# Kernel optimization log

Measured on AMD Instinct MI355X. Metric: run time of the kernel, lower is better.

Reference implementation:

```python
import jax, jax.numpy as jnp
import numpy as np

EPS = 1e-5  # BatchNorm2d default eps


def conv1x1_bn(x, W, gamma, beta, mean, var):
    # 1x1 conv (no bias) + BatchNorm2d in inference form.
    # x: (n, Cin, h, w), W: (Cout, Cin)
    y = jnp.einsum('oc,nchw->nohw', W, x)
    inv = gamma / jnp.sqrt(var + EPS)          # (C,)
    return y * inv[None, :, None, None] + (beta - mean * inv)[None, :, None, None]


def setup_inputs() -> dict:
    key = jax.random.key(0)
    ks = jax.random.split(key, 16)
    B, C, H, W = 8, 256, 128, 128
    sd = 1.0 / np.sqrt(C)
    inp = {
        'x':  jax.random.normal(ks[0], (B, C, H, W), jnp.float32),
        'Wk': jax.random.normal(ks[1], (C, C), jnp.float32) * sd,
        'k_gamma': jax.random.uniform(ks[2], (C,), jnp.float32, 0.5, 1.5),
        'k_beta':  jax.random.normal(ks[3], (C,), jnp.float32) * 0.1,
        'k_mean':  jax.random.normal(ks[4], (C,), jnp.float32) * 0.1,
        'k_var':   jax.random.uniform(ks[5], (C,), jnp.float32, 0.5, 1.5),
        'Wq': jax.random.normal(ks[6], (C, C), jnp.float32) * sd,
        'q_gamma': jax.random.uniform(ks[7], (C,), jnp.float32, 0.5, 1.5),
        'q_beta':  jax.random.normal(ks[8], (C,), jnp.float32) * 0.1,
        'q_mean':  jax.random.normal(ks[9], (C,), jnp.float32) * 0.1,
        'q_var':   jax.random.uniform(ks[10], (C,), jnp.float32, 0.5, 1.5),
        'Wv': jax.random.normal(ks[11], (C, C), jnp.float32) * sd,
        'v_gamma': jax.random.uniform(ks[12], (C,), jnp.float32, 0.5, 1.5),
        'v_beta':  jax.random.normal(ks[13], (C,), jnp.float32) * 0.1,
        'v_mean':  jax.random.normal(ks[14], (C,), jnp.float32) * 0.1,
        'v_var':   jax.random.uniform(ks[15], (C,), jnp.float32, 0.5, 1.5),
    }
    return inp


def reference(x, Wk, k_gamma, k_beta, k_mean, k_var,
              Wq, q_gamma, q_beta, q_mean, q_var,
              Wv, v_gamma, v_beta, v_mean, v_var):
    n, c, h, w = x.shape
    k = conv1x1_bn(x, Wk, k_gamma, k_beta, k_mean, k_var).reshape(n, c, h * w)  # (n,C,S)
    q = conv1x1_bn(x, Wq, q_gamma, q_beta, q_mean, q_var).reshape(n, c, h * w)
    v = conv1x1_bn(x, Wv, v_gamma, v_beta, v_mean, v_var).reshape(n, c, h * w)
    # torch: attention = softmax(q @ k^T, dim=2) -> (n, C, C) channel attention
    attn = jax.nn.softmax(jnp.einsum('ncs,nds->ncd', q, k), axis=-1)
    out = jnp.einsum('ncd,nds->ncs', attn, v).reshape(n, c, h, w)
    return out + x  # res = Identity (in_channels == out_channels)
```

## Files before the change

### kernel.cpp

```cpp
#include <hip/hip_runtime.h>


typedef __bf16 bf16x8 __attribute__((ext_vector_type(8)));
typedef float f32x4 __attribute__((ext_vector_type(4)));
typedef unsigned short us8 __attribute__((ext_vector_type(8)));

#define EPS 1e-5f

__device__ __forceinline__ unsigned short f2bf(float f) {
  unsigned int u = __float_as_uint(f);
  u += 0x7fffu + ((u >> 16) & 1u);
  return (unsigned short)(u >> 16);
}
__device__ __forceinline__ float bf2f(unsigned short h) {
  return __uint_as_float(((unsigned int)h) << 16);
}
__device__ __forceinline__ bf16x8 ld_frag(const unsigned short* p) {
  union { us8 u; bf16x8 b; } x;
  x.u = *(const us8*)p;
  return x.b;
}

#define LDBS 40

#define CONV_WRITE                                                          \
  _Pragma("unroll")                                                         \
  for (int u = 0; u < 4; ++u) {                                             \
    float fv[8] = {pa[u].x, pa[u].y, pa[u].z, pa[u].w,                      \
                   pb[u].x, pb[u].y, pb[u].z, pb[u].w};                     \
    union { unsigned short s[8]; uint4 v; } H, L;                           \
    _Pragma("unroll")                                                       \
    for (int e = 0; e < 8; ++e) {                                           \
      const unsigned short hh = f2bf(fv[e]);                                \
      H.s[e] = hh;                                                          \
      L.s[e] = f2bf(2.0f * (fv[e] - bf2f(hh)));                             \
      rs[u] += fv[e];                                                       \
    }                                                                       \
    *(uint4*)&sh[(srow + u * 64) * LDBS + sg * 8] = H.v;                    \
    *(uint4*)&sl[(srow + u * 64) * LDBS + sg * 8] = L.v;                    \
  }

__global__ __launch_bounds__(256, 2) void kGram(const float* __restrict__ x,
                                                float* __restrict__ Gp,
                                                float* __restrict__ rp,
                                                int chunk) {
  __shared__ __align__(16) unsigned short sh[256 * LDBS];
  __shared__ __align__(16) unsigned short sl[256 * LDBS];
  const int n = blockIdx.z, h = blockIdx.y;
  const int k0 = blockIdx.x * chunk;
  const int nkt = chunk >> 5;
  const int tid = threadIdx.x;
  const float* xn = x + (size_t)n * 4194304;

  f32x4 acc[4][8];
  const f32x4 z4 = {0.f, 0.f, 0.f, 0.f};
#pragma unroll
  for (int i = 0; i < 4; ++i)
#pragma unroll
    for (int j = 0; j < 8; ++j) acc[i][j] = z4;
  float rs[4] = {0.f, 0.f, 0.f, 0.f};

  const int lane = tid & 63, w = tid >> 6;
  const int m = lane & 15, q = lane >> 4;
  const int wr = w >> 1, wc = w & 1;
  const int srow = tid >> 2, sg = tid & 3;

  float4 pa[4], pb[4];

#pragma unroll
  for (int u = 0; u < 4; ++u) {
    const float* p = xn + (size_t)(srow + u * 64) * 16384 + k0 + sg * 8;
    pa[u] = *(const float4*)p;
    pb[u] = *(const float4*)(p + 4);
  }

  for (int kt = 0; kt < nkt; ++kt) {
    if (kt) __syncthreads();
    CONV_WRITE
    __syncthreads();
    if (kt + 1 < nkt) {
      const int kb = k0 + (kt + 1) * 32;
#pragma unroll
      for (int u = 0; u < 4; ++u) {
        const float* p = xn + (size_t)(srow + u * 64) * 16384 + kb + sg * 8;
        pa[u] = *(const float4*)p;
        pb[u] = *(const float4*)(p + 4);
      }
    }
    bf16x8 Ah[4];
#pragma unroll
    for (int i = 0; i < 4; ++i)
      Ah[i] = ld_frag(&sh[(h * 128 + wr * 64 + i * 16 + m) * LDBS + q * 8]);
#pragma unroll
    for (int j = 0; j < 8; ++j) {
      const int off = (wc * 128 + j * 16 + m) * LDBS + q * 8;
      const bf16x8 Bh = ld_frag(&sh[off]);
      const bf16x8 Bl = ld_frag(&sl[off]);
#pragma unroll
      for (int i = 0; i < 4; ++i) {
        acc[i][j] = __builtin_amdgcn_mfma_f32_16x16x32_bf16(Ah[i], Bh, acc[i][j], 0, 0, 0);
        acc[i][j] = __builtin_amdgcn_mfma_f32_16x16x32_bf16(Ah[i], Bl, acc[i][j], 0, 0, 0);
      }
    }
  }

  const size_t slot = (size_t)n * gridDim.x + blockIdx.x;
  if (h == 0) {
#pragma unroll
    for (int u = 0; u < 4; ++u) {
      float v = rs[u];
      v += __shfl_xor(v, 1);
      v += __shfl_xor(v, 2);
      if ((lane & 3) == 0) rp[slot * 256 + (srow + u * 64)] = v;
    }
  }
  float* Gpn = Gp + slot * 65536;
#pragma unroll
  for (int i = 0; i < 4; ++i)
#pragma unroll
    for (int j = 0; j < 8; ++j)
#pragma unroll
      for (int e = 0; e < 4; ++e) {
        const int grow = h * 128 + wr * 64 + i * 16 + q * 4 + e;
        const int gcol = wc * 128 + j * 16 + m;
        Gpn[grow * 256 + gcol] = 0.5f * acc[i][j][e];
      }
}

__global__ void kReduce(float* __restrict__ Gp, int splits) {
  const int e4 = (blockIdx.x * 256 + threadIdx.x) * 4;
  const int n = e4 >> 16, el = e4 & 65535;
  float* p = Gp + (size_t)n * splits * 65536 + el;
  float4 s = {0.f, 0.f, 0.f, 0.f};
  for (int i = 0; i < splits; ++i) {
    const float4 v = *(const float4*)(p + (size_t)i * 65536);
    s.x += v.x; s.y += v.y; s.z += v.z; s.w += v.w;
  }
  *(float4*)p = s;
}

__global__ void kSym(const float* __restrict__ Gs, float* __restrict__ G,
                     int sstride) {
  __shared__ __align__(16) float pt[64][68];
  const int n = blockIdx.y;
  const int bi = blockIdx.x >> 2, bj = blockIdx.x & 3;
  const float* gsn = Gs + (size_t)n * sstride;
  float* gn = G + (size_t)n * 65536;
  const int t = threadIdx.x, r = t >> 2, cg = (t & 3) * 16;
#pragma unroll
  for (int e = 0; e < 16; e += 4)
    *(float4*)&pt[r][cg + e] =
        *(const float4*)(gsn + (size_t)(bj * 64 + r) * 256 + bi * 64 + cg + e);
  __syncthreads();
#pragma unroll
  for (int e = 0; e < 16; e += 4) {
    const float4 a =
        *(const float4*)(gsn + (size_t)(bi * 64 + r) * 256 + bj * 64 + cg + e);
    float4 o;
    o.x = a.x + pt[cg + e + 0][r];
    o.y = a.y + pt[cg + e + 1][r];
    o.z = a.z + pt[cg + e + 2][r];
    o.w = a.w + pt[cg + e + 3][r];
    *(float4*)(gn + (size_t)(bi * 64 + r) * 256 + bj * 64 + cg + e) = o;
  }
}

#define TLD 260
__global__ __launch_bounds__(256) void kAttn(
    const float* __restrict__ G, const float* __restrict__ rp, int splits,
    const float* __restrict__ Wq, const float* __restrict__ qga, const float* __restrict__ qbe,
    const float* __restrict__ qme, const float* __restrict__ qva,
    const float* __restrict__ Wk, const float* __restrict__ kga, const float* __restrict__ kbe,
    const float* __restrict__ kme, const float* __restrict__ kva,
    const float* __restrict__ Wv, const float* __restrict__ vga, const float* __restrict__ vbe,
    const float* __restrict__ vme, const float* __restrict__ vva,
    unsigned short* __restrict__ M, float* __restrict__ cvec) {
  __shared__ __align__(16) float t_lds[8 * TLD];
  __shared__ __align__(16) float p_lds[8 * TLD];
  __shared__ __align__(16) float r_lds[256];
  __shared__ float ivv_lds[256], bv_lds[256];
  __shared__ float rq_lds[8], bq_lds[8], rsum_lds[8];

  const int n = blockIdx.y, r0 = blockIdx.x * 8;
  const int t = threadIdx.x;
  const int lane = t & 63;
  const int w = __builtin_amdgcn_readfirstlane(t >> 6);
  const float* Gn = G + (size_t)n * 65536;

  {
    float s = 0.f;
    const float* p = rp + (size_t)n * splits * 256 + t;
    for (int ss = 0; ss < splits; ++ss) s += p[ss * 256];
    r_lds[t] = s;
    const float iv = vga[t] * rsqrtf(vva[t] + EPS);
    ivv_lds[t] = iv;
    bv_lds[t] = vbe[t] - vme[t] * iv;
  }
  __syncthreads();

  const int c0 = r0 + 2 * w, c1 = c0 + 1;
  const float ivq0 = qga[c0] * rsqrtf(qva[c0] + EPS);
  const float ivq1 = qga[c1] * rsqrtf(qva[c1] + EPS);

  {
    const float4 r4 = *(const float4*)(r_lds + lane * 4);
#pragma unroll
    for (int rr = 0; rr < 2; ++rr) {
      const float4 w4 = *(const float4*)(Wq + (size_t)(c0 + rr) * 256 + lane * 4);
      float s = w4.x * r4.x + w4.y * r4.y + w4.z * r4.z + w4.w * r4.w;
      s += __shfl_xor(s, 1);  s += __shfl_xor(s, 2);  s += __shfl_xor(s, 4);
      s += __shfl_xor(s, 8);  s += __shfl_xor(s, 16); s += __shfl_xor(s, 32);
      if (lane == 0) rq_lds[2 * w + rr] = s * (rr ? ivq1 : ivq0);
    }
    if (lane == 0) {
      bq_lds[2 * w + 0] = qbe[c0] - qme[c0] * ivq0;
      bq_lds[2 * w + 1] = qbe[c1] - qme[c1] * ivq1;
    }
  }

  {
    float4 tr0 = {0.f, 0.f, 0.f, 0.f}, tr1 = {0.f, 0.f, 0.f, 0.f};
    const float* wq0 = Wq + (size_t)c0 * 256;
    const float* wq1 = Wq + (size_t)c1 * 256;
    for (int kb = 0; kb < 256; kb += 4) {
      union { float4 v; float f[4]; } A0, A1;
      A0.v = *(const float4*)(wq0 + kb);
      A1.v = *(const float4*)(wq1 + kb);
#pragma unroll
      for (int e = 0; e < 4; ++e) {
        const float4 g4 = *(const float4*)(Gn + (size_t)(kb + e) * 256 + lane * 4);
        const float a0 = A0.f[e], a1 = A1.f[e];
        tr0.x += a0 * g4.x; tr0.y += a0 * g4.y; tr0.z += a0 * g4.z; tr0.w += a0 * g4.w;
        tr1.x += a1 * g4.x; tr1.y += a1 * g4.y; tr1.z += a1 * g4.z; tr1.w += a1 * g4.w;
      }
    }
    tr0.x *= ivq0; tr0.y *= ivq0; tr0.z *= ivq0; tr0.w *= ivq0;
    tr1.x *= ivq1; tr1.y *= ivq1; tr1.z *= ivq1; tr1.w *= ivq1;
    *(float4*)(t_lds + (2 * w + 0) * TLD + lane * 4) = tr0;
    *(float4*)(t_lds + (2 * w + 1) * TLD + lane * 4) = tr1;
  }
  __syncthreads();

  {
    float lreg[8];
#pragma unroll
    for (int i = 0; i < 8; ++i) lreg[i] = 0.f;
    const float ivk = kga[t] * rsqrtf(kva[t] + EPS);
    const float bkd = kbe[t] - kme[t] * ivk;
    float rkd = 0.f;
    const float* wkrow = Wk + (size_t)t * 256;
    for (int jb = 0; jb < 256; jb += 4) {
      const float4 w4 = *(const float4*)(wkrow + jb);
      const float4 r4 = *(const float4*)(r_lds + jb);
      rkd += w4.x * r4.x + w4.y * r4.y + w4.z * r4.z + w4.w * r4.w;
#pragma unroll
      for (int i = 0; i < 8; ++i) {
        const float4 t4 = *(const float4*)(t_lds + i * TLD + jb);
        lreg[i] += t4.x * w4.x + t4.y * w4.y + t4.z * w4.z + t4.w * w4.w;
      }
    }
#pragma unroll
    for (int i = 0; i < 8; ++i)
      p_lds[i * TLD + t] = ivk * lreg[i] + rq_lds[i] * bkd +
                           bq_lds[i] * (ivk * rkd) + 16384.0f * bq_lds[i] * bkd;
  }
  __syncthreads();

  {
    const int i = t >> 5, s = t & 31;
    float* row = p_lds + i * TLD;
    float mx = -1e30f;
#pragma unroll
    for (int u = 0; u < 8; ++u) mx = fmaxf(mx, row[s + u * 32]);
    mx = fmaxf(mx, __shfl_xor(mx, 1));
    mx = fmaxf(mx, __shfl_xor(mx, 2));
    mx = fmaxf(mx, __shfl_xor(mx, 4));
    mx = fmaxf(mx, __shfl_xor(mx, 8));
    mx = fmaxf(mx, __shfl_xor(mx, 16));
    float sraw = 0.f, sbv = 0.f;
#pragma unroll
    for (int u = 0; u < 8; ++u) {
      const int d = s + u * 32;
      const float e = __expf(row[d] - mx);
      sraw += e;
      sbv += e * bv_lds[d];
      row[d] = e * ivv_lds[d];
    }
    sraw += __shfl_xor(sraw, 1);  sbv += __shfl_xor(sbv, 1);
    sraw += __shfl_xor(sraw, 2);  sbv += __shfl_xor(sbv, 2);
    sraw += __shfl_xor(sraw, 4);  sbv += __shfl_xor(sbv, 4);
    sraw += __shfl_xor(sraw, 8);  sbv += __shfl_xor(sbv, 8);
    sraw += __shfl_xor(sraw, 16); sbv += __shfl_xor(sbv, 16);
    if (s == 0) {
      rsum_lds[i] = sraw;
      cvec[n * 256 + r0 + i] = sbv / sraw;
    }
  }
  __syncthreads();

  {
    float mreg[8];
#pragma unroll
    for (int i = 0; i < 8; ++i) mreg[i] = 0.f;
    for (int db = 0; db < 256; db += 4) {
      float wv[4];
#pragma unroll
      for (int e = 0; e < 4; ++e) wv[e] = Wv[(size_t)(db + e) * 256 + t];
#pragma unroll
      for (int i = 0; i < 8; ++i) {
        const float4 p4 = *(const float4*)(p_lds + i * TLD + db);
        mreg[i] += p4.x * wv[0] + p4.y * wv[1] + p4.z * wv[2] + p4.w * wv[3];
      }
    }
#pragma unroll
    for (int i = 0; i < 8; ++i)
      M[((size_t)n * 256 + r0 + i) * 256 + t] = f2bf(mreg[i] / rsum_lds[i]);
  }
}

#define LDT 40
__global__ __launch_bounds__(256, 2) void kOut(const float* __restrict__ x,
                                               const unsigned short* __restrict__ M,
                                               const float* __restrict__ cvec,
                                               float* __restrict__ out) {
  __shared__ __align__(16) unsigned short xt[64 * LDT];
  __shared__ __align__(16) float xf[256 * 64];
  const int n = blockIdx.y, s0 = blockIdx.x * 64;
  const int tid = threadIdx.x;
  const float* xn = x + (size_t)n * 4194304;
  const unsigned short* Mn = M + (size_t)n * 65536;
  const int lane = tid & 63, w = tid >> 6;
  const int m = lane & 15, q = lane >> 4;
  const int ch0 = tid >> 4, f0 = tid & 15;

  f32x4 acc[4][4];
  const f32x4 z4 = {0.f, 0.f, 0.f, 0.f};
#pragma unroll
  for (int i = 0; i < 4; ++i)
#pragma unroll
    for (int ct = 0; ct < 4; ++ct) acc[i][ct] = z4;

  float4 pv[2];
#pragma unroll
  for (int u = 0; u < 2; ++u)
    pv[u] = *(const float4*)(xn + (size_t)(ch0 + u * 16) * 16384 + s0 + f0 * 4);

  for (int kt = 0; kt < 8; ++kt) {
    if (kt) __syncthreads();
#pragma unroll
    for (int u = 0; u < 2; ++u) {
      const int ch = kt * 32 + ch0 + u * 16;
      const float4 v = pv[u];
      *(float4*)&xf[ch * 64 + f0 * 4] = v;
      xt[(f0 * 4 + 0) * LDT + ch - kt * 32] = f2bf(v.x);
      xt[(f0 * 4 + 1) * LDT + ch - kt * 32] = f2bf(v.y);
      xt[(f0 * 4 + 2) * LDT + ch - kt * 32] = f2bf(v.z);
      xt[(f0 * 4 + 3) * LDT + ch - kt * 32] = f2bf(v.w);
    }
    bf16x8 A[4];
#pragma unroll
    for (int i = 0; i < 4; ++i)
      A[i] = ld_frag(&Mn[((w * 4 + i) * 16 + m) * 256 + kt * 32 + q * 8]);
    __syncthreads();
    if (kt < 7) {
#pragma unroll
      for (int u = 0; u < 2; ++u)
        pv[u] = *(const float4*)(xn + (size_t)((kt + 1) * 32 + ch0 + u * 16) * 16384 + s0 + f0 * 4);
    }
    bf16x8 B[4];
#pragma unroll
    for (int ct = 0; ct < 4; ++ct)
      B[ct] = ld_frag(&xt[(ct * 16 + m) * LDT + q * 8]);
#pragma unroll
    for (int i = 0; i < 4; ++i)
#pragma unroll
      for (int ct = 0; ct < 4; ++ct)
        acc[i][ct] = __builtin_amdgcn_mfma_f32_16x16x32_bf16(A[i], B[ct], acc[i][ct], 0, 0, 0);
  }
#pragma unroll
  for (int i = 0; i < 4; ++i) {
    const int cb = w * 64 + i * 16 + q * 4;
#pragma unroll
    for (int e = 0; e < 4; ++e) {
      const int c = cb + e;
      const float cv = cvec[n * 256 + c];
      float* orow = out + ((size_t)n * 256 + c) * 16384 + s0;
#pragma unroll
      for (int ct = 0; ct < 4; ++ct) {
        const int s = ct * 16 + m;
        orow[s] = acc[i][ct][e] + cv + xf[c * 64 + s];
      }
    }
  }
}

extern "C" void kernel_launch(void* const* d_in, const int* in_sizes, int n_in,
                              void* d_out, int out_size, void* d_ws, size_t ws_size,
                              hipStream_t stream) {
  const float* x   = (const float*)d_in[0];
  const float* Wk  = (const float*)d_in[1];
  const float* kga = (const float*)d_in[2];
  const float* kbe = (const float*)d_in[3];
  const float* kme = (const float*)d_in[4];
  const float* kva = (const float*)d_in[5];
  const float* Wq  = (const float*)d_in[6];
  const float* qga = (const float*)d_in[7];
  const float* qbe = (const float*)d_in[8];
  const float* qme = (const float*)d_in[9];
  const float* qva = (const float*)d_in[10];
  const float* Wv  = (const float*)d_in[11];
  const float* vga = (const float*)d_in[12];
  const float* vbe = (const float*)d_in[13];
  const float* vme = (const float*)d_in[14];
  const float* vva = (const float*)d_in[15];

  char* ws = (char*)d_ws;
  float* G           = (float*)(ws);
  unsigned short* Mm = (unsigned short*)(ws + 2097152);
  float* cv          = (float*)(ws + 3145728);
  float* rp          = (float*)(ws + 3153920);
  float* Gp          = (float*)(ws + 3416064);
  float* out         = (float*)d_out;

  int splits = 32;
  while (splits > 1 &&
         (size_t)3416064 + (size_t)splits * 8 * 65536 * 4 > ws_size)
    splits >>= 1;
  const int chunk = 16384 / splits;

  kGram<<<dim3(splits, 2, 8), 256, 0, stream>>>(x, Gp, rp, chunk);
  kReduce<<<512, 256, 0, stream>>>(Gp, splits);
  kSym<<<dim3(16, 8), 256, 0, stream>>>(Gp, G, splits * 65536);
  kAttn<<<dim3(32, 8), 256, 0, stream>>>(G, rp, splits,
                                         Wq, qga, qbe, qme, qva,
                                         Wk, kga, kbe, kme, kva,
                                         Wv, vga, vbe, vme, vva,
                                         Mm, cv);
  kOut<<<dim3(256, 8), 256, 0, stream>>>(x, Mm, cv, out);
}
```

Measured before the change: 388.1 us.

## Fuse split reduction with symmetrization, halve attention rows per block, vectorize output stores

Merges the split-sum reduction and the transpose-add symmetrization into a single kernel that walks only upper-triangular 64x64 tile pairs, removing one launch and one full pass over the partial Gram buffer. The attention kernel now handles 4 rows per block instead of 8, doubling the grid to improve occupancy, at the cost of more redundant loads of G, Wk and Wv. The output kernel swaps the MFMA operand order so each lane holds 4 consecutive spatial positions, allowing float4 stores and float4 residual reads. The fused reduce uses only 80 blocks, each serially summing all splits, so it has less parallelism than the old 512-block reduction.

```diff
diff --git a/kernel.cpp b/kernel.cpp
--- a/kernel.cpp
+++ b/kernel.cpp
@@ -127,41 +127,60 @@
       }
 }
 
-__global__ void kReduce(float* __restrict__ Gp, int splits) {
-  const int e4 = (blockIdx.x * 256 + threadIdx.x) * 4;
-  const int n = e4 >> 16, el = e4 & 65535;
-  float* p = Gp + (size_t)n * splits * 65536 + el;
-  float4 s = {0.f, 0.f, 0.f, 0.f};
-  for (int i = 0; i < splits; ++i) {
-    const float4 v = *(const float4*)(p + (size_t)i * 65536);
-    s.x += v.x; s.y += v.y; s.z += v.z; s.w += v.w;
-  }
-  *(float4*)p = s;
-}
-
-__global__ void kSym(const float* __restrict__ Gs, float* __restrict__ G,
-                     int sstride) {
-  __shared__ __align__(16) float pt[64][68];
-  const int n = blockIdx.y;
-  const int bi = blockIdx.x >> 2, bj = blockIdx.x & 3;
-  const float* gsn = Gs + (size_t)n * sstride;
+__global__ void kRedSym(const float* __restrict__ Gp, float* __restrict__ G,
+                        int splits) {
+  __shared__ __align__(16) float tl[64][68];
+  const int n = blockIdx.y, p = blockIdx.x;
+  const int bi = p < 4 ? 0 : p < 7 ? 1 : p < 9 ? 2 : 3;
+  const int bj = p < 4 ? p : p < 7 ? p - 3 : p < 9 ? p - 5 : 3;
+  const int t = threadIdx.x, r = t >> 2, cg = (t & 3) * 16;
+  float a[16], b[16];
+#pragma unroll
+  for (int e = 0; e < 16; ++e) { a[e] = 0.f; b[e] = 0.f; }
+  const float* base = Gp + (size_t)n * splits * 65536;
+  for (int s = 0; s < splits; ++s) {
+    const float* ps = base + (size_t)s * 65536;
+#pragma unroll
+    for (int e = 0; e < 16; e += 4) {
+      const float4 va = *(const float4*)(ps + (size_t)(bi * 64 + r) * 256 + bj * 64 + cg + e);
+      a[e] += va.x; a[e + 1] += va.y; a[e + 2] += va.z; a[e + 3] += va.w;
+      if (bi != bj) {
+        const float4 vb = *(const float4*)(ps + (size_t)(bj * 64 + r) * 256 + bi * 64 + cg + e);
+        b[e] += vb.x; b[e + 1] += vb.y; b[e + 2] += vb.z; b[e + 3] += vb.w;
+      }
+    }
+  }
+  if (bi == bj) {
+#pragma unroll
+    for (int e = 0; e < 16; ++e) b[e] = a[e];
+  }
   float* gn = G + (size_t)n * 65536;
-  const int t = threadIdx.x, r = t >> 2, cg = (t & 3) * 16;
-#pragma unroll
-  for (int e = 0; e < 16; e += 4)
-    *(float4*)&pt[r][cg + e] =
-        *(const float4*)(gsn + (size_t)(bj * 64 + r) * 256 + bi * 64 + cg + e);
+#pragma unroll
+  for (int e = 0; e < 16; ++e) tl[r][cg + e] = b[e];
   __syncthreads();
 #pragma unroll
   for (int e = 0; e < 16; e += 4) {
-    const float4 a =
-        *(const float4*)(gsn + (size_t)(bi * 64 + r) * 256 + bj * 64 + cg + e);
     float4 o;
-    o.x = a.x + pt[cg + e + 0][r];
-    o.y = a.y + pt[cg + e + 1][r];
-    o.z = a.z + pt[cg + e + 2][r];
-    o.w = a.w + pt[cg + e + 3][r];
+    o.x = a[e + 0] + tl[cg + e + 0][r];
+    o.y = a[e + 1] + tl[cg + e + 1][r];
+    o.z = a[e + 2] + tl[cg + e + 2][r];
+    o.w = a[e + 3] + tl[cg + e + 3][r];
     *(float4*)(gn + (size_t)(bi * 64 + r) * 256 + bj * 64 + cg + e) = o;
+  }
+  if (bi != bj) {
+    __syncthreads();
+#pragma unroll
+    for (int e = 0; e < 16; ++e) tl[r][cg + e] = a[e];
+    __syncthreads();
+#pragma unroll
+    for (int e = 0; e < 16; e += 4) {
+      float4 o;
+      o.x = b[e + 0] + tl[cg + e + 0][r];
+      o.y = b[e + 1] + tl[cg + e + 1][r];
+      o.z = b[e + 2] + tl[cg + e + 2][r];
+      o.w = b[e + 3] + tl[cg + e + 3][r];
+      *(float4*)(gn + (size_t)(bj * 64 + r) * 256 + bi * 64 + cg + e) = o;
+    }
   }
 }
 
@@ -175,13 +194,13 @@
     const float* __restrict__ Wv, const float* __restrict__ vga, const float* __restrict__ vbe,
     const float* __restrict__ vme, const float* __restrict__ vva,
     unsigned short* __restrict__ M, float* __restrict__ cvec) {
-  __shared__ __align__(16) float t_lds[8 * TLD];
-  __shared__ __align__(16) float p_lds[8 * TLD];
+  __shared__ __align__(16) float t_lds[4 * TLD];
+  __shared__ __align__(16) float p_lds[4 * TLD];
   __shared__ __align__(16) float r_lds[256];
   __shared__ float ivv_lds[256], bv_lds[256];
-  __shared__ float rq_lds[8], bq_lds[8], rsum_lds[8];
-
-  const int n = blockIdx.y, r0 = blockIdx.x * 8;
+  __shared__ float rq_lds[4], bq_lds[4], rsum_lds[4];
+
+  const int n = blockIdx.y, r0 = blockIdx.x * 4;
   const int t = threadIdx.x;
   const int lane = t & 63;
   const int w = __builtin_amdgcn_readfirstlane(t >> 6);
@@ -198,53 +217,43 @@
   }
   __syncthreads();
 
-  const int c0 = r0 + 2 * w, c1 = c0 + 1;
+  const int c0 = r0 + w;
   const float ivq0 = qga[c0] * rsqrtf(qva[c0] + EPS);
-  const float ivq1 = qga[c1] * rsqrtf(qva[c1] + EPS);
 
   {
     const float4 r4 = *(const float4*)(r_lds + lane * 4);
-#pragma unroll
-    for (int rr = 0; rr < 2; ++rr) {
-      const float4 w4 = *(const float4*)(Wq + (size_t)(c0 + rr) * 256 + lane * 4);
-      float s = w4.x * r4.x + w4.y * r4.y + w4.z * r4.z + w4.w * r4.w;
-      s += __shfl_xor(s, 1);  s += __shfl_xor(s, 2);  s += __shfl_xor(s, 4);
-      s += __shfl_xor(s, 8);  s += __shfl_xor(s, 16); s += __shfl_xor(s, 32);
-      if (lane == 0) rq_lds[2 * w + rr] = s * (rr ? ivq1 : ivq0);
-    }
+    const float4 w4 = *(const float4*)(Wq + (size_t)c0 * 256 + lane * 4);
+    float s = w4.x * r4.x + w4.y * r4.y + w4.z * r4.z + w4.w * r4.w;
+    s += __shfl_xor(s, 1);  s += __shfl_xor(s, 2);  s += __shfl_xor(s, 4);
+    s += __shfl_xor(s, 8);  s += __shfl_xor(s, 16); s += __shfl_xor(s, 32);
     if (lane == 0) {
-      bq_lds[2 * w + 0] = qbe[c0] - qme[c0] * ivq0;
-      bq_lds[2 * w + 1] = qbe[c1] - qme[c1] * ivq1;
-    }
-  }
-
-  {
-    float4 tr0 = {0.f, 0.f, 0.f, 0.f}, tr1 = {0.f, 0.f, 0.f, 0.f};
+      rq_lds[w] = s * ivq0;
+      bq_lds[w] = qbe[c0] - qme[c0] * ivq0;
+    }
+  }
+
+  {
+    float4 tr0 = {0.f, 0.f, 0.f, 0.f};
     const float* wq0 = Wq + (size_t)c0 * 256;
-    const float* wq1 = Wq + (size_t)c1 * 256;
     for (int kb = 0; kb < 256; kb += 4) {
-      union { float4 v; float f[4]; } A0, A1;
+      union { float4 v; float f[4]; } A0;
       A0.v = *(const float4*)(wq0 + kb);
-      A1.v = *(const float4*)(wq1 + kb);
 #pragma unroll
       for (int e = 0; e < 4; ++e) {
         const float4 g4 = *(const float4*)(Gn + (size_t)(kb + e) * 256 + lane * 4);
-        const float a0 = A0.f[e], a1 = A1.f[e];
+        const float a0 = A0.f[e];
         tr0.x += a0 * g4.x; tr0.y += a0 * g4.y; tr0.z += a0 * g4.z; tr0.w += a0 * g4.w;
-        tr1.x += a1 * g4.x; tr1.y += a1 * g4.y; tr1.z += a1 * g4.z; tr1.w += a1 * g4.w;
       }
     }
     tr0.x *= ivq0; tr0.y *= ivq0; tr0.z *= ivq0; tr0.w *= ivq0;
-    tr1.x *= ivq1; tr1.y *= ivq1; tr1.z *= ivq1; tr1.w *= ivq1;
-    *(float4*)(t_lds + (2 * w + 0) * TLD + lane * 4) = tr0;
-    *(float4*)(t_lds + (2 * w + 1) * TLD + lane * 4) = tr1;
+    *(float4*)(t_lds + w * TLD + lane * 4) = tr0;
   }
   __syncthreads();
 
   {
-    float lreg[8];
-#pragma unroll
-    for (int i = 0; i < 8; ++i) lreg[i] = 0.f;
+    float lreg[4];
+#pragma unroll
+    for (int i = 0; i < 4; ++i) lreg[i] = 0.f;
     const float ivk = kga[t] * rsqrtf(kva[t] + EPS);
     const float bkd = kbe[t] - kme[t] * ivk;
     float rkd = 0.f;
@@ -254,33 +263,34 @@
       const float4 r4 = *(const float4*)(r_lds + jb);
       rkd += w4.x * r4.x + w4.y * r4.y + w4.z * r4.z + w4.w * r4.w;
 #pragma unroll
-      for (int i = 0; i < 8; ++i) {
+      for (int i = 0; i < 4; ++i) {
         const float4 t4 = *(const float4*)(t_lds + i * TLD + jb);
         lreg[i] += t4.x * w4.x + t4.y * w4.y + t4.z * w4.z + t4.w * w4.w;
       }
     }
 #pragma unroll
-    for (int i = 0; i < 8; ++i)
+    for (int i = 0; i < 4; ++i)
       p_lds[i * TLD + t] = ivk * lreg[i] + rq_lds[i] * bkd +
                            bq_lds[i] * (ivk * rkd) + 16384.0f * bq_lds[i] * bkd;
   }
   __syncthreads();
 
   {
-    const int i = t >> 5, s = t & 31;
+    const int i = t >> 6, s = t & 63;
     float* row = p_lds + i * TLD;
     float mx = -1e30f;
 #pragma unroll
-    for (int u = 0; u < 8; ++u) mx = fmaxf(mx, row[s + u * 32]);
+    for (int u = 0; u < 4; ++u) mx = fmaxf(mx, row[s + u * 64]);
     mx = fmaxf(mx, __shfl_xor(mx, 1));
     mx = fmaxf(mx, __shfl_xor(mx, 2));
     mx = fmaxf(mx, __shfl_xor(mx, 4));
     mx = fmaxf(mx, __shfl_xor(mx, 8));
     mx = fmaxf(mx, __shfl_xor(mx, 16));
+    mx = fmaxf(mx, __shfl_xor(mx, 32));
     float sraw = 0.f, sbv = 0.f;
 #pragma unroll
-    for (int u = 0; u < 8; ++u) {
-      const int d = s + u * 32;
+    for (int u = 0; u < 4; ++u) {
+      const int d = s + u * 64;
       const float e = __expf(row[d] - mx);
       sraw += e;
       sbv += e * bv_lds[d];
@@ -291,6 +301,7 @@
     sraw += __shfl_xor(sraw, 4);  sbv += __shfl_xor(sbv, 4);
     sraw += __shfl_xor(sraw, 8);  sbv += __shfl_xor(sbv, 8);
     sraw += __shfl_xor(sraw, 16); sbv += __shfl_xor(sbv, 16);
+    sraw += __shfl_xor(sraw, 32); sbv += __shfl_xor(sbv, 32);
     if (s == 0) {
       rsum_lds[i] = sraw;
       cvec[n * 256 + r0 + i] = sbv / sraw;
@@ -299,21 +310,21 @@
   __syncthreads();
 
   {
-    float mreg[8];
-#pragma unroll
-    for (int i = 0; i < 8; ++i) mreg[i] = 0.f;
+    float mreg[4];
+#pragma unroll
+    for (int i = 0; i < 4; ++i) mreg[i] = 0.f;
     for (int db = 0; db < 256; db += 4) {
       float wv[4];
 #pragma unroll
       for (int e = 0; e < 4; ++e) wv[e] = Wv[(size_t)(db + e) * 256 + t];
 #pragma unroll
-      for (int i = 0; i < 8; ++i) {
+      for (int i = 0; i < 4; ++i) {
         const float4 p4 = *(const float4*)(p_lds + i * TLD + db);
         mreg[i] += p4.x * wv[0] + p4.y * wv[1] + p4.z * wv[2] + p4.w * wv[3];
       }
     }
 #pragma unroll
-    for (int i = 0; i < 8; ++i)
+    for (int i = 0; i < 4; ++i)
       M[((size_t)n * 256 + r0 + i) * 256 + t] = f2bf(mreg[i] / rsum_lds[i]);
   }
 }
@@ -375,21 +386,23 @@
     for (int i = 0; i < 4; ++i)
 #pragma unroll
       for (int ct = 0; ct < 4; ++ct)
-        acc[i][ct] = __builtin_amdgcn_mfma_f32_16x16x32_bf16(A[i], B[ct], acc[i][ct], 0, 0, 0);
+        acc[i][ct] = __builtin_amdgcn_mfma_f32_16x16x32_bf16(B[ct], A[i], acc[i][ct], 0, 0, 0);
   }
 #pragma unroll
   for (int i = 0; i < 4; ++i) {
-    const int cb = w * 64 + i * 16 + q * 4;
-#pragma unroll
-    for (int e = 0; e < 4; ++e) {
-      const int c = cb + e;
-      const float cv = cvec[n * 256 + c];
-      float* orow = out + ((size_t)n * 256 + c) * 16384 + s0;
-#pragma unroll
-      for (int ct = 0; ct < 4; ++ct) {
-        const int s = ct * 16 + m;
-        orow[s] = acc[i][ct][e] + cv + xf[c * 64 + s];
-      }
+    const int c = (w * 4 + i) * 16 + m;
+    const float cv = cvec[n * 256 + c];
+    float* orow = out + ((size_t)n * 256 + c) * 16384 + s0;
+#pragma unroll
+    for (int ct = 0; ct < 4; ++ct) {
+      const int sl = ct * 16 + q * 4;
+      const float4 xr = *(const float4*)&xf[c * 64 + sl];
+      float4 o;
+      o.x = acc[i][ct][0] + cv + xr.x;
+      o.y = acc[i][ct][1] + cv + xr.y;
+      o.z = acc[i][ct][2] + cv + xr.z;
+      o.w = acc[i][ct][3] + cv + xr.w;
+      *(float4*)(orow + sl) = o;
     }
   }
 }
@@ -429,9 +442,8 @@
   const int chunk = 16384 / splits;
 
   kGram<<<dim3(splits, 2, 8), 256, 0, stream>>>(x, Gp, rp, chunk);
-  kReduce<<<512, 256, 0, stream>>>(Gp, splits);
-  kSym<<<dim3(16, 8), 256, 0, stream>>>(Gp, G, splits * 65536);
-  kAttn<<<dim3(32, 8), 256, 0, stream>>>(G, rp, splits,
+  kRedSym<<<dim3(10, 8), 256, 0, stream>>>(Gp, G, splits);
+  kAttn<<<dim3(64, 8), 256, 0, stream>>>(G, rp, splits,
                                          Wq, qga, qbe, qme, qva,
                                          Wk, kga, kbe, kme, kva,
                                          Wv, vga, vbe, vme, vva,
```

Measured after the change: 420.8 us. 8.4% more time.
